# Kernel tuning notes

Hardware: AMD Instinct MI355X
Metric: run time of the kernel (lower is better)

## Reference

```python
import jax, jax.numpy as jnp
import numpy as np

NUM_HEADS = 16
HEAD_DIM = 128
ROPE_BASE = 10000.0


def _rotate_half(x):
    x1, x2 = jnp.split(x, 2, axis=-1)
    return jnp.concatenate([-x2, x1], axis=-1)


def setup_inputs() -> dict:
    key = jax.random.key(0)
    ks = jax.random.split(key, 6)
    B, S, H = 2, 2048, 2048
    hidden_states = jax.random.normal(ks[0], (B, S, H), dtype=jnp.float32)
    # causal additive mask: 0 on/below diagonal, large negative above
    causal = jnp.tril(jnp.ones((S, S), dtype=bool))
    attention_mask = jnp.where(causal, 0.0, -1e9).astype(jnp.float32)[None, None]
    position_ids = jnp.broadcast_to(jnp.arange(S, dtype=jnp.int64), (B, S))
    sc = 1.0 / np.sqrt(H)
    Wq = jax.random.normal(ks[1], (H, H), dtype=jnp.float32) * sc
    Wk = jax.random.normal(ks[2], (H, H), dtype=jnp.float32) * sc
    Wv = jax.random.normal(ks[3], (H, H), dtype=jnp.float32) * sc
    Wo = jax.random.normal(ks[4], (H, H), dtype=jnp.float32) * sc
    return {"hidden_states": hidden_states, "attention_mask": attention_mask,
            "position_ids": position_ids, "Wq": Wq, "Wk": Wk, "Wv": Wv, "Wo": Wo}


def reference(hidden_states, attention_mask, position_ids, Wq, Wk, Wv, Wo):
    B, S, H = hidden_states.shape
    nH, hd = NUM_HEADS, HEAD_DIM
    # projections (torch Linear: x @ W.T)
    q = (hidden_states @ Wq.T).reshape(B, S, nH, hd).transpose(0, 2, 1, 3)  # [B,nH,S,hd]
    k = (hidden_states @ Wk.T).reshape(B, S, nH, hd).transpose(0, 2, 1, 3)
    v = (hidden_states @ Wv.T).reshape(B, S, nH, hd).transpose(0, 2, 1, 3)
    # rotary embeddings: cos/sin cache over positions, duplicated to full head_dim
    inv_freq = 1.0 / (ROPE_BASE ** (jnp.arange(0, hd, 2, dtype=jnp.float32) / hd))  # [hd/2]
    t = jnp.arange(S, dtype=jnp.float32)
    freqs = jnp.outer(t, inv_freq)                       # [S, hd/2]
    emb = jnp.concatenate([freqs, freqs], axis=-1)       # [S, hd]
    cos = jnp.cos(emb)[position_ids][:, None]            # [B,1,S,hd]
    sin = jnp.sin(emb)[position_ids][:, None]
    q = q * cos + _rotate_half(q) * sin
    k = k * cos + _rotate_half(k) * sin
    # eager attention
    scores = jnp.einsum('bhqd,bhkd->bhqk', q, k) / np.sqrt(hd).astype(np.float32)
    scores = scores + attention_mask
    attn = jax.nn.softmax(scores, axis=-1)
    out = jnp.einsum('bhqk,bhkd->bhqd', attn, v)         # [B,nH,S,hd]
    out = out.transpose(0, 2, 1, 3).reshape(B, S, H)
    return out @ Wo.T
```

## Files before the change

### kernel.cpp

```cpp
#include <hip/hip_runtime.h>
#include <cstdint>
#include <cstddef>

#define NH    16
#define HD    128
#define SEQ   2048
#define HID   2048
#define BATCH 2
#define MTOT  (BATCH*SEQ)

#define SCALE 0.08838834764831845f
#define L2E   1.4426950408889634f
#define KSCL  (0.08838834764831845f * 1.4426950408889634f)

typedef __bf16 bf16x8 __attribute__((ext_vector_type(8)));
typedef float  floatx4 __attribute__((ext_vector_type(4)));

__device__ __forceinline__ unsigned short f2bf(float f) {
  union { float f; unsigned u; } v; v.f = f;
  unsigned u = v.u;
  return (unsigned short)((u + 0x7FFFu + ((u >> 16) & 1u)) >> 16);
}

__device__ __forceinline__ void gld16(const unsigned short* g, unsigned short* l) {
  auto gp = reinterpret_cast<const __attribute__((address_space(1))) void*>(
      reinterpret_cast<uintptr_t>(g));
  auto lp = reinterpret_cast<__attribute__((address_space(3))) void*>(
      reinterpret_cast<uintptr_t>(l));
  __builtin_amdgcn_global_load_lds(gp, lp, 16, 0, 0);
}

__global__ void cvt_f32_bf16(const float* __restrict__ src,
                             unsigned short* __restrict__ dst, int n4) {
  int i = blockIdx.x * blockDim.x + threadIdx.x;
  if (i >= n4) return;
  float4 v = reinterpret_cast<const float4*>(src)[i];
  ushort4 o;
  o.x = f2bf(v.x); o.y = f2bf(v.y); o.z = f2bf(v.z); o.w = f2bf(v.w);
  reinterpret_cast<ushort4*>(dst)[i] = o;
}

__global__ void rope_table(float2* __restrict__ tab) {
  int idx = blockIdx.x * blockDim.x + threadIdx.x;
  if (idx >= SEQ * 64) return;
  int pos = idx >> 6, i = idx & 63;
  double freq = pow(10000.0, -(double)(2 * i) / 128.0);
  double th = (double)pos * freq;
  tab[idx] = make_float2((float)cos(th), (float)sin(th));
}

__device__ __forceinline__ int noff(int wn, int t) {
  return wn * 32 + (t & 1) * 16 + (t >> 1) * 64;
}

__device__ __forceinline__ void gemm_core(const unsigned short* __restrict__ A,
                                          const unsigned short* __restrict__ B,
                                          int K, int mBase, int nBase,
                                          unsigned short* As, unsigned short* Bs,
                                          floatx4 acc[4][4]) {
  int tid  = threadIdx.x;
  int wave = tid >> 6, lane = tid & 63;
  int l16  = lane & 15, quad = lane >> 4;
  int wm   = wave >> 1, wn = wave & 1;

  const unsigned short* Ag = A + (size_t)mBase * K;
  const unsigned short* Bg = B + (size_t)nBase * K;

  for (int k0 = 0; k0 < K; k0 += 32) {
    __syncthreads();
#pragma unroll
    for (int r = 0; r < 2; ++r) {
      int row0 = wave * 32 + r * 16;
      int grow = row0 + (lane >> 2);
      int gcol = k0 + (lane & 3) * 8;
      gld16(Ag + (size_t)grow * K + gcol, As + row0 * 32 + lane * 8);
      gld16(Bg + (size_t)grow * K + gcol, Bs + row0 * 32 + lane * 8);
    }
    __syncthreads();

    bf16x8 af[4], bfr[4];
#pragma unroll
    for (int t = 0; t < 4; ++t) {
      af[t]  = *reinterpret_cast<const bf16x8*>(&As[(wm * 64 + t * 16 + l16) * 32 + quad * 8]);
      bfr[t] = *reinterpret_cast<const bf16x8*>(&Bs[(noff(wn, t) + l16) * 32 + quad * 8]);
    }
#pragma unroll
    for (int tm = 0; tm < 4; ++tm)
#pragma unroll
      for (int tn = 0; tn < 4; ++tn)
        acc[tm][tn] = __builtin_amdgcn_mfma_f32_16x16x32_bf16(af[tm], bfr[tn], acc[tm][tn], 0, 0, 0);
  }
}

__global__ __launch_bounds__(256)
void gemm_qkv(const unsigned short* __restrict__ Xb,
              const unsigned short* __restrict__ Wq,
              const unsigned short* __restrict__ Wk,
              const unsigned short* __restrict__ Wv,
              const float2* __restrict__ tab,
              unsigned short* __restrict__ Qo,
              unsigned short* __restrict__ Ko,
              unsigned short* __restrict__ Vto) {
  __shared__ unsigned short As[128 * 32];
  __shared__ unsigned short Bs[128 * 32];
  int z = blockIdx.z;
  const unsigned short* W = (z == 0) ? Wq : (z == 1) ? Wk : Wv;
  int mBase = blockIdx.y * 128, nBase = blockIdx.x * 128;

  floatx4 acc[4][4];
#pragma unroll
  for (int i = 0; i < 4; ++i)
#pragma unroll
    for (int j = 0; j < 4; ++j) acc[i][j] = {0.f, 0.f, 0.f, 0.f};

  gemm_core(Xb, W, HID, mBase, nBase, As, Bs, acc);

  int tid = threadIdx.x;
  int wave = tid >> 6, lane = tid & 63;
  int l16 = lane & 15, quad = lane >> 4;
  int wm = wave >> 1, wn = wave & 1;
  int hh = nBase >> 7;

#pragma unroll
  for (int tm = 0; tm < 4; ++tm) {
    int mrow = mBase + wm * 64 + tm * 16 + quad * 4;
    if (z < 2) {
      unsigned short* dst = (z == 0) ? Qo : Ko;
#pragma unroll
      for (int p = 0; p < 2; ++p) {
        int dlo = wn * 32 + p * 16 + l16;
#pragma unroll
        for (int r = 0; r < 4; ++r) {
          int m = mrow + r;
          int bb = m >> 11, s = m & (SEQ - 1);
          float2 cs = tab[s * 64 + dlo];
          float a = acc[tm][p][r], bv = acc[tm][p + 2][r];
          size_t base = (((size_t)bb * NH + hh) * SEQ + s) * HD;
          dst[base + dlo]      = f2bf(a * cs.x - bv * cs.y);
          dst[base + dlo + 64] = f2bf(bv * cs.x + a * cs.y);
        }
      }
    } else {
      int bb = mrow >> 11, s = mrow & (SEQ - 1);
#pragma unroll
      for (int tn = 0; tn < 4; ++tn) {
        int d = noff(wn, tn) + l16;
        ushort4 pk;
        pk.x = f2bf(acc[tm][tn][0]); pk.y = f2bf(acc[tm][tn][1]);
        pk.z = f2bf(acc[tm][tn][2]); pk.w = f2bf(acc[tm][tn][3]);
        *reinterpret_cast<ushort4*>(&Vto[(((size_t)bb * NH + hh) * HD + d) * SEQ + s]) = pk;
      }
    }
  }
}

__global__ __launch_bounds__(256)
void gemm_out(const unsigned short* __restrict__ Ob,
              const unsigned short* __restrict__ Wo,
              float* __restrict__ out) {
  __shared__ unsigned short As[128 * 32];
  __shared__ unsigned short Bs[128 * 32];
  int mBase = blockIdx.y * 128, nBase = blockIdx.x * 128;

  floatx4 acc[4][4];
#pragma unroll
  for (int i = 0; i < 4; ++i)
#pragma unroll
    for (int j = 0; j < 4; ++j) acc[i][j] = {0.f, 0.f, 0.f, 0.f};

  gemm_core(Ob, Wo, HID, mBase, nBase, As, Bs, acc);

  int tid = threadIdx.x;
  int wave = tid >> 6, lane = tid & 63;
  int l16 = lane & 15, quad = lane >> 4;
  int wm = wave >> 1, wn = wave & 1;

#pragma unroll
  for (int tm = 0; tm < 4; ++tm) {
    int mrow = mBase + wm * 64 + tm * 16 + quad * 4;
#pragma unroll
    for (int tn = 0; tn < 4; ++tn) {
      int n = nBase + noff(wn, tn) + l16;
#pragma unroll
      for (int r = 0; r < 4; ++r)
        out[(size_t)(mrow + r) * HID + n] = acc[tm][tn][r];
    }
  }
}

__global__ __launch_bounds__(512)
void attn_kernel(const unsigned short* __restrict__ Q,
                 const unsigned short* __restrict__ K,
                 const unsigned short* __restrict__ Vt,
                 unsigned short* __restrict__ Ob) {
  __shared__ unsigned short Ks[32 * 136];
  __shared__ unsigned short Vs[128 * 40];
  __shared__ unsigned short Ps[8][16 * 40];

  int qt = 15 - blockIdx.y;
  int bh = blockIdx.x;
  int b = bh >> 4, h = bh & 15;
  int q0 = qt * 128;
  int tid = threadIdx.x;
  int wave = tid >> 6, lane = tid & 63;
  int l16 = lane & 15, quad = lane >> 4;

  const size_t headQ = (size_t)bh * SEQ * HD;
  const size_t headV = (size_t)bh * HD * SEQ;

  bf16x8 qf[4];
  {
    int qrow = q0 + wave * 16 + l16;
    const unsigned short* qp = Q + headQ + (size_t)qrow * HD + quad * 8;
#pragma unroll
    for (int c = 0; c < 4; ++c)
      qf[c] = *reinterpret_cast<const bf16x8*>(qp + c * 32);
  }

  floatx4 oacc[8];
#pragma unroll
  for (int i = 0; i < 8; ++i) oacc[i] = {0.f, 0.f, 0.f, 0.f};
  float rs[4];
#pragma unroll
  for (int r = 0; r < 4; ++r) rs[r] = 0.f;

  int qq = q0 + wave * 16 + quad * 4;
  int qmax = q0 + wave * 16 + 15;
  unsigned short* pw = Ps[wave];

  int nkt = q0 / 32 + 4;
  for (int kt = 0; kt < nkt; ++kt) {
    int k0 = kt * 32;
    __syncthreads();
    {
      int row = tid >> 4, dc = (tid & 15) * 8;
      *reinterpret_cast<uint4*>(&Ks[row * 136 + dc]) =
        *reinterpret_cast<const uint4*>(&K[headQ + (size_t)(k0 + row) * HD + dc]);
    }
    {
      int row = tid >> 2, kc = (tid & 3) * 8;
      *reinterpret_cast<uint4*>(&Vs[row * 40 + kc]) =
        *reinterpret_cast<const uint4*>(&Vt[headV + (size_t)row * SEQ + k0 + kc]);
    }
    __syncthreads();

    if (k0 <= qmax) {
      floatx4 sc[2];
#pragma unroll
      for (int nt = 0; nt < 2; ++nt) {
        floatx4 s4 = {0.f, 0.f, 0.f, 0.f};
#pragma unroll
        for (int c = 0; c < 4; ++c) {
          bf16x8 kf = *reinterpret_cast<const bf16x8*>(&Ks[(nt * 16 + l16) * 136 + c * 32 + quad * 8]);
          s4 = __builtin_amdgcn_mfma_f32_16x16x32_bf16(qf[c], kf, s4, 0, 0, 0);
        }
        sc[nt] = s4;
      }

#pragma unroll
      for (int nt = 0; nt < 2; ++nt) {
        int kk = k0 + nt * 16 + l16;
#pragma unroll
        for (int r = 0; r < 4; ++r) {
          float arg = (kk <= qq + r) ? fmaf(sc[nt][r], KSCL, -32.0f) : -1e9f;
          float p = exp2f(arg);
          rs[r] += p;
          pw[(quad * 4 + r) * 40 + nt * 16 + l16] = f2bf(p);
        }
      }
      __asm__ __volatile__("s_waitcnt lgkmcnt(0)" ::: "memory");
      bf16x8 pf = *reinterpret_cast<const bf16x8*>(&pw[l16 * 40 + quad * 8]);

#pragma unroll
      for (int dt = 0; dt < 8; ++dt) {
        bf16x8 vf = *reinterpret_cast<const bf16x8*>(&Vs[(dt * 16 + l16) * 40 + quad * 8]);
        oacc[dt] = __builtin_amdgcn_mfma_f32_16x16x32_bf16(pf, vf, oacc[dt], 0, 0, 0);
      }
    }
  }

#pragma unroll
  for (int off = 1; off < 16; off <<= 1)
#pragma unroll
    for (int r = 0; r < 4; ++r) rs[r] += __shfl_xor(rs[r], off, 16);

  float inv[4];
#pragma unroll
  for (int r = 0; r < 4; ++r) inv[r] = 1.0f / rs[r];
#pragma unroll
  for (int dt = 0; dt < 8; ++dt)
#pragma unroll
    for (int r = 0; r < 4; ++r) {
      int s = q0 + wave * 16 + quad * 4 + r;
      Ob[(((size_t)b * SEQ + s) * NH + h) * HD + dt * 16 + l16] = f2bf(oacc[dt][r] * inv[r]);
    }
}

extern "C" void kernel_launch(void* const* d_in, const int* in_sizes, int n_in,
                              void* d_out, int out_size, void* d_ws, size_t ws_size,
                              hipStream_t stream) {
  const float* X  = (const float*)d_in[0];
  const float* Wq = (const float*)d_in[3];
  const float* Wk = (const float*)d_in[4];
  const float* Wv = (const float*)d_in[5];
  const float* Wo = (const float*)d_in[6];

  char* w = (char*)d_ws;
  size_t off = 0;
  auto alloc = [&](size_t bytes) { char* p = w + off; off += (bytes + 255) & ~(size_t)255; return p; };

  unsigned short* Xb  = (unsigned short*)alloc((size_t)MTOT * HID * 2);
  unsigned short* Wqb = (unsigned short*)alloc((size_t)HID * HID * 2);
  unsigned short* Wkb = (unsigned short*)alloc((size_t)HID * HID * 2);
  unsigned short* Wvb = (unsigned short*)alloc((size_t)HID * HID * 2);
  unsigned short* Wob = (unsigned short*)alloc((size_t)HID * HID * 2);
  unsigned short* Qb  = (unsigned short*)alloc((size_t)BATCH * NH * SEQ * HD * 2);
  unsigned short* Kb  = (unsigned short*)alloc((size_t)BATCH * NH * SEQ * HD * 2);
  unsigned short* Vtb = (unsigned short*)alloc((size_t)BATCH * NH * HD * SEQ * 2);
  unsigned short* Obf = (unsigned short*)alloc((size_t)BATCH * SEQ * NH * HD * 2);
  float2*         tab = (float2*)alloc((size_t)SEQ * 64 * sizeof(float2));

  const int nX4 = (MTOT * HID) / 4;
  const int nW4 = (HID * HID) / 4;
  rope_table<<<(SEQ * 64 + 255) / 256, 256, 0, stream>>>(tab);
  cvt_f32_bf16<<<(nX4 + 255) / 256, 256, 0, stream>>>(X, Xb, nX4);
  cvt_f32_bf16<<<(nW4 + 255) / 256, 256, 0, stream>>>(Wq, Wqb, nW4);
  cvt_f32_bf16<<<(nW4 + 255) / 256, 256, 0, stream>>>(Wk, Wkb, nW4);
  cvt_f32_bf16<<<(nW4 + 255) / 256, 256, 0, stream>>>(Wv, Wvb, nW4);
  cvt_f32_bf16<<<(nW4 + 255) / 256, 256, 0, stream>>>(Wo, Wob, nW4);

  gemm_qkv<<<dim3(HID / 128, MTOT / 128, 3), 256, 0, stream>>>(Xb, Wqb, Wkb, Wvb, tab, Qb, Kb, Vtb);

  attn_kernel<<<dim3(BATCH * NH, SEQ / 128), 512, 0, stream>>>(Qb, Kb, Vtb, Obf);

  gemm_out<<<dim3(HID / 128, MTOT / 128), 256, 0, stream>>>(Obf, Wob, (float*)d_out);
}
```

Baseline: 439.9 us.

## Merge conversion kernels, move RoPE into separate pass, simplify GEMM tile mapping

Combines the five fp32-to-bf16 conversion launches into one kernel and drops the precomputed RoPE table. The GEMM now writes unrotated Q/K, and a new in-place rope_qk kernel applies the rotation using float exp2/sin/cos. The interleaved noff column mapping is replaced with contiguous per-wave columns. This trades fewer launches and a simpler epilogue for an extra read-modify-write pass over Q and K. It also adds an extra bf16 rounding of Q/K before rotation and uses lower-precision float trig.

```diff
diff --git a/kernel.cpp b/kernel.cpp
--- a/kernel.cpp
+++ b/kernel.cpp
@@ -12,6 +12,7 @@
 #define SCALE 0.08838834764831845f
 #define L2E   1.4426950408889634f
 #define KSCL  (0.08838834764831845f * 1.4426950408889634f)
+#define L2_10K_D64 0.20762050593046458f
 
 typedef __bf16 bf16x8 __attribute__((ext_vector_type(8)));
 typedef float  floatx4 __attribute__((ext_vector_type(4)));
@@ -20,6 +21,9 @@
   union { float f; unsigned u; } v; v.f = f;
   unsigned u = v.u;
   return (unsigned short)((u + 0x7FFFu + ((u >> 16) & 1u)) >> 16);
+}
+__device__ __forceinline__ float bf2f(unsigned short h) {
+  union { unsigned u; float f; } v; v.u = ((unsigned)h) << 16; return v.f;
 }
 
 __device__ __forceinline__ void gld16(const unsigned short* g, unsigned short* l) {
@@ -30,27 +34,44 @@
   __builtin_amdgcn_global_load_lds(gp, lp, 16, 0, 0);
 }
 
-__global__ void cvt_f32_bf16(const float* __restrict__ src,
-                             unsigned short* __restrict__ dst, int n4) {
+__global__ void cvt_all(const float* __restrict__ X,
+                        const float* __restrict__ Wq, const float* __restrict__ Wk,
+                        const float* __restrict__ Wv, const float* __restrict__ Wo,
+                        unsigned short* __restrict__ Xb,
+                        unsigned short* __restrict__ Wqb, unsigned short* __restrict__ Wkb,
+                        unsigned short* __restrict__ Wvb, unsigned short* __restrict__ Wob) {
   int i = blockIdx.x * blockDim.x + threadIdx.x;
-  if (i >= n4) return;
-  float4 v = reinterpret_cast<const float4*>(src)[i];
+  const float* src; unsigned short* dst; int k;
+  if (i < (1 << 21)) { src = X; dst = Xb; k = i; }
+  else {
+    int j = i - (1 << 21);
+    int seg = j >> 20; k = j & ((1 << 20) - 1);
+    src = (seg == 0) ? Wq : (seg == 1) ? Wk : (seg == 2) ? Wv : Wo;
+    dst = (seg == 0) ? Wqb : (seg == 1) ? Wkb : (seg == 2) ? Wvb : Wob;
+  }
+  float4 v = reinterpret_cast<const float4*>(src)[k];
   ushort4 o;
   o.x = f2bf(v.x); o.y = f2bf(v.y); o.z = f2bf(v.z); o.w = f2bf(v.w);
-  reinterpret_cast<ushort4*>(dst)[i] = o;
-}
-
-__global__ void rope_table(float2* __restrict__ tab) {
+  reinterpret_cast<ushort4*>(dst)[k] = o;
+}
+
+__global__ void rope_qk(unsigned short* __restrict__ Q,
+                        unsigned short* __restrict__ Kk) {
   int idx = blockIdx.x * blockDim.x + threadIdx.x;
-  if (idx >= SEQ * 64) return;
-  int pos = idx >> 6, i = idx & 63;
-  double freq = pow(10000.0, -(double)(2 * i) / 128.0);
-  double th = (double)pos * freq;
-  tab[idx] = make_float2((float)cos(th), (float)sin(th));
-}
-
-__device__ __forceinline__ int noff(int wn, int t) {
-  return wn * 32 + (t & 1) * 16 + (t >> 1) * 64;
+  if (idx >= BATCH * NH * SEQ * 64) return;
+  int i  = idx & 63;
+  int s  = (idx >> 6) & (SEQ - 1);
+  int bh = idx >> 17;
+  float freq = exp2f(-(float)i * L2_10K_D64);
+  float th = (float)s * freq;
+  float cx = cosf(th), sy = sinf(th);
+  size_t base = ((size_t)bh * SEQ + s) * HD;
+  float qa = bf2f(Q[base + i]), qb = bf2f(Q[base + i + 64]);
+  Q[base + i]      = f2bf(qa * cx - qb * sy);
+  Q[base + i + 64] = f2bf(qb * cx + qa * sy);
+  float ka = bf2f(Kk[base + i]), kb = bf2f(Kk[base + i + 64]);
+  Kk[base + i]      = f2bf(ka * cx - kb * sy);
+  Kk[base + i + 64] = f2bf(kb * cx + ka * sy);
 }
 
 __device__ __forceinline__ void gemm_core(const unsigned short* __restrict__ A,
@@ -82,7 +103,7 @@
 #pragma unroll
     for (int t = 0; t < 4; ++t) {
       af[t]  = *reinterpret_cast<const bf16x8*>(&As[(wm * 64 + t * 16 + l16) * 32 + quad * 8]);
-      bfr[t] = *reinterpret_cast<const bf16x8*>(&Bs[(noff(wn, t) + l16) * 32 + quad * 8]);
+      bfr[t] = *reinterpret_cast<const bf16x8*>(&Bs[(wn * 64 + t * 16 + l16) * 32 + quad * 8]);
     }
 #pragma unroll
     for (int tm = 0; tm < 4; ++tm)
@@ -97,7 +118,6 @@
               const unsigned short* __restrict__ Wq,
               const unsigned short* __restrict__ Wk,
               const unsigned short* __restrict__ Wv,
-              const float2* __restrict__ tab,
               unsigned short* __restrict__ Qo,
               unsigned short* __restrict__ Ko,
               unsigned short* __restrict__ Vto) {
@@ -119,32 +139,24 @@
   int wave = tid >> 6, lane = tid & 63;
   int l16 = lane & 15, quad = lane >> 4;
   int wm = wave >> 1, wn = wave & 1;
-  int hh = nBase >> 7;
 
 #pragma unroll
   for (int tm = 0; tm < 4; ++tm) {
     int mrow = mBase + wm * 64 + tm * 16 + quad * 4;
-    if (z < 2) {
-      unsigned short* dst = (z == 0) ? Qo : Ko;
-#pragma unroll
-      for (int p = 0; p < 2; ++p) {
-        int dlo = wn * 32 + p * 16 + l16;
+#pragma unroll
+    for (int tn = 0; tn < 4; ++tn) {
+      int n = nBase + wn * 64 + tn * 16 + l16;
+      int hh = n >> 7, d = n & 127;
+      if (z < 2) {
+        unsigned short* dst = (z == 0) ? Qo : Ko;
 #pragma unroll
         for (int r = 0; r < 4; ++r) {
           int m = mrow + r;
           int bb = m >> 11, s = m & (SEQ - 1);
-          float2 cs = tab[s * 64 + dlo];
-          float a = acc[tm][p][r], bv = acc[tm][p + 2][r];
-          size_t base = (((size_t)bb * NH + hh) * SEQ + s) * HD;
-          dst[base + dlo]      = f2bf(a * cs.x - bv * cs.y);
-          dst[base + dlo + 64] = f2bf(bv * cs.x + a * cs.y);
+          dst[(((size_t)bb * NH + hh) * SEQ + s) * HD + d] = f2bf(acc[tm][tn][r]);
         }
-      }
-    } else {
-      int bb = mrow >> 11, s = mrow & (SEQ - 1);
-#pragma unroll
-      for (int tn = 0; tn < 4; ++tn) {
-        int d = noff(wn, tn) + l16;
+      } else {
+        int bb = mrow >> 11, s = mrow & (SEQ - 1);
         ushort4 pk;
         pk.x = f2bf(acc[tm][tn][0]); pk.y = f2bf(acc[tm][tn][1]);
         pk.z = f2bf(acc[tm][tn][2]); pk.w = f2bf(acc[tm][tn][3]);
@@ -180,7 +192,7 @@
     int mrow = mBase + wm * 64 + tm * 16 + quad * 4;
 #pragma unroll
     for (int tn = 0; tn < 4; ++tn) {
-      int n = nBase + noff(wn, tn) + l16;
+      int n = nBase + wn * 64 + tn * 16 + l16;
 #pragma unroll
       for (int r = 0; r < 4; ++r)
         out[(size_t)(mrow + r) * HID + n] = acc[tm][tn][r];
@@ -318,18 +330,13 @@
   unsigned short* Kb  = (unsigned short*)alloc((size_t)BATCH * NH * SEQ * HD * 2);
   unsigned short* Vtb = (unsigned short*)alloc((size_t)BATCH * NH * HD * SEQ * 2);
   unsigned short* Obf = (unsigned short*)alloc((size_t)BATCH * SEQ * NH * HD * 2);
-  float2*         tab = (float2*)alloc((size_t)SEQ * 64 * sizeof(float2));
-
-  const int nX4 = (MTOT * HID) / 4;
-  const int nW4 = (HID * HID) / 4;
-  rope_table<<<(SEQ * 64 + 255) / 256, 256, 0, stream>>>(tab);
-  cvt_f32_bf16<<<(nX4 + 255) / 256, 256, 0, stream>>>(X, Xb, nX4);
-  cvt_f32_bf16<<<(nW4 + 255) / 256, 256, 0, stream>>>(Wq, Wqb, nW4);
-  cvt_f32_bf16<<<(nW4 + 255) / 256, 256, 0, stream>>>(Wk, Wkb, nW4);
-  cvt_f32_bf16<<<(nW4 + 255) / 256, 256, 0, stream>>>(Wv, Wvb, nW4);
-  cvt_f32_bf16<<<(nW4 + 255) / 256, 256, 0, stream>>>(Wo, Wob, nW4);
-
-  gemm_qkv<<<dim3(HID / 128, MTOT / 128, 3), 256, 0, stream>>>(Xb, Wqb, Wkb, Wvb, tab, Qb, Kb, Vtb);
+
+  const int nAll4 = (MTOT * HID + 4 * HID * HID) / 4;
+  cvt_all<<<nAll4 / 256, 256, 0, stream>>>(X, Wq, Wk, Wv, Wo, Xb, Wqb, Wkb, Wvb, Wob);
+
+  gemm_qkv<<<dim3(HID / 128, MTOT / 128, 3), 256, 0, stream>>>(Xb, Wqb, Wkb, Wvb, Qb, Kb, Vtb);
+
+  rope_qk<<<(BATCH * NH * SEQ * 64) / 256, 256, 0, stream>>>(Qb, Kb);
 
   attn_kernel<<<dim3(BATCH * NH, SEQ / 128), 512, 0, stream>>>(Qb, Kb, Vtb, Obf);
 
```

Result: faster. 414.5 us (-5.8%).
